# Kernel tuning notes

Hardware: AMD Instinct MI355X
Metric: run time of the kernel (lower is better)

Reference implementation:

```python
import jax, jax.numpy as jnp
import numpy as np

K = 3
LOSS_WEIGHT = 1.0
EPS_NORM = 1e-8
EPS_DIV = 1e-10


def setup_inputs() -> dict:
    key = jax.random.key(0)
    k1, k2, k3 = jax.random.split(key, 3)
    N = 32768          # total points over all segments
    NSEG = 8           # number of scenes (len(nums)); equal-size segments of 4096
    pred_ = jax.random.normal(k1, (N, 3), dtype=jnp.float32)
    coord = jax.random.uniform(k2, (N, 3), dtype=jnp.float32) * 10.0
    target = jax.random.normal(k3, (N, 3), dtype=jnp.float32)
    nums = jnp.arange(NSEG, dtype=jnp.int32)  # only len(nums) matters; segments are equal-sized
    return {"pred_": pred_, "coord": coord, "target": target, "nums": nums}


def _segment_loss(cp, pp, tp):
    # cp: (S,3) coords, pp: (S,3) normalized pred, tp: (S,3) target
    # squared euclidean distances via the ||x||^2 trick (monotone in distance,
    # so topk-smallest matches torch.cdist + topk(largest=False))
    sq = jnp.sum(cp * cp, axis=-1)                       # (S,)
    d2 = sq[:, None] + sq[None, :] - 2.0 * (cp @ cp.T)   # (S,S)
    S = cp.shape[0]
    eye = jnp.eye(S, dtype=bool)
    d2 = jnp.where(eye, -1.0, jnp.maximum(d2, 0.0))      # self always nearest
    _, idx = jax.lax.top_k(-d2, K + 1)                   # (S,K+1) smallest dists
    idx = idx[:, 1:]                                     # drop self -> (S,K)

    nbr = pp[idx]                                        # (S,K,3) gather
    sim = jnp.abs(jnp.sum(nbr * pp[:, None, :], axis=2))
    sim = jnp.clip(sim, -1.0, 1.0)

    tnbr = tp[idx]                                       # (S,K,3)
    tsim = jnp.abs(jnp.sum(tnbr * tp[:, None, :], axis=2))
    tsim = jnp.clip(tsim, -1.0, 1.0)

    return jnp.mean((sim - tsim) ** 2)                   # F.mse_loss(mean)


def reference(pred_, coord, target, nums):
    nseg = nums.shape[0]
    seg = pred_.shape[0] // nseg
    # normalize predicted directions
    inp = jnp.sqrt(jnp.sum(pred_ * pred_, axis=-1, keepdims=True) + EPS_NORM)
    pred_norm = pred_ / (inp + EPS_DIV)
    c = coord.reshape(nseg, seg, 3)
    p = pred_norm.reshape(nseg, seg, 3)
    t = target.reshape(nseg, seg, 3)
    losses = jax.vmap(_segment_loss)(c, p, t)            # (nseg,)
    return jnp.mean(losses) * LOSS_WEIGHT
```

## Files before the change

kernel.cpp:

```cpp
#include <hip/hip_runtime.h>
#include <math.h>

#define G 8
#define NCELL (G*G*G)
#define INV_CS 0.8f
#define CS 1.25f
#define KNN 3
#define BIGF 3.402823466e+38f

#define BUILD_BLOCK 1024
#define SEARCH_BLOCK 512
#define SPLIT 8
#define PTS_PER_SBLOCK (SEARCH_BLOCK / SPLIT)

__device__ __forceinline__ int cell_of(float x, float y, float z) {
    int cx = (int)(x * INV_CS); cx = cx < 0 ? 0 : (cx > G-1 ? G-1 : cx);
    int cy = (int)(y * INV_CS); cy = cy < 0 ? 0 : (cy > G-1 ? G-1 : cy);
    int cz = (int)(z * INV_CS); cz = cz < 0 ? 0 : (cz > G-1 ? G-1 : cz);
    return (cx << 6) | (cy << 3) | cz;
}

__device__ __forceinline__ void pk_insert(double pk, double& m0, double& m1, double& m2) {
    const double lo0 = fmin(m0, pk);
    const double hi0 = fmax(m0, pk);
    m0 = lo0;
    const double lo1 = fmin(m1, hi0);
    const double hi1 = fmax(m1, hi0);
    m1 = lo1;
    m2 = fmin(m2, hi1);
}

__global__ __launch_bounds__(BUILD_BLOCK) void build_grid(
    const float* __restrict__ coord,
    float4* __restrict__ sorted,
    int* __restrict__ cellstart,
    float* __restrict__ out,
    int seg)
{
    __shared__ int hist[NCELL];
    __shared__ int scanb[NCELL];
    __shared__ int start[NCELL + 1];

    const int tid = threadIdx.x;
    const int s   = blockIdx.x;
    const long segbase = (long)s * seg;

    if (s == 0 && tid == 0) out[0] = 0.0f;

    if (tid < NCELL) hist[tid] = 0;
    __syncthreads();

    for (int p = tid; p < seg; p += BUILD_BLOCK) {
        const float x = coord[(segbase + p)*3 + 0];
        const float y = coord[(segbase + p)*3 + 1];
        const float z = coord[(segbase + p)*3 + 2];
        atomicAdd(&hist[cell_of(x, y, z)], 1);
    }
    __syncthreads();

    if (tid < NCELL) scanb[tid] = hist[tid];
    __syncthreads();
    for (int off = 1; off < NCELL; off <<= 1) {
        int add = 0;
        if (tid < NCELL && tid >= off) add = scanb[tid - off];
        __syncthreads();
        if (tid < NCELL) scanb[tid] += add;
        __syncthreads();
    }
    if (tid < NCELL) {
        start[tid] = scanb[tid] - hist[tid];
        if (tid == NCELL - 1) start[NCELL] = scanb[tid];
    }
    __syncthreads();

    if (tid < NCELL) {
        cellstart[s * (NCELL + 1) + tid] = start[tid];
        if (tid == 0) cellstart[s * (NCELL + 1) + NCELL] = start[NCELL];
        hist[tid] = start[tid];
    }
    __syncthreads();

    for (int p = tid; p < seg; p += BUILD_BLOCK) {
        const float x = coord[(segbase + p)*3 + 0];
        const float y = coord[(segbase + p)*3 + 1];
        const float z = coord[(segbase + p)*3 + 2];
        const int c = cell_of(x, y, z);
        const int slot = atomicAdd(&hist[c], 1);
        sorted[segbase + slot] = make_float4(x, y, z, __int_as_float(p));
    }
}

__global__ __launch_bounds__(SEARCH_BLOCK) void knn_loss(
    const float4* __restrict__ sorted,
    const int* __restrict__ cellstart,
    const float* __restrict__ pred,
    const float* __restrict__ target,
    float* __restrict__ out,
    int seg, float inv_total)
{
    __shared__ int csl[NCELL + 1];
    __shared__ float wred[SEARCH_BLOCK / 64];

    const int tid = threadIdx.x;
    const int sub = tid & (SPLIT - 1);
    const int pt  = blockIdx.x * PTS_PER_SBLOCK + (tid >> 3);
    const int s   = pt >> 12;
    const int j   = pt & 4095;
    const long segbase = (long)s * seg;

    for (int i = tid; i < NCELL + 1; i += SEARCH_BLOCK)
        csl[i] = cellstart[s * (NCELL + 1) + i];
    __syncthreads();

    const float4 me = sorted[segbase + j];
    const int myorig = __float_as_int(me.w);
    const int cx = (me.x * INV_CS) > (float)(G-1) ? G-1 : (int)(me.x * INV_CS);
    const int cy = (me.y * INV_CS) > (float)(G-1) ? G-1 : (int)(me.y * INV_CS);
    const int cz = (me.z * INV_CS) > (float)(G-1) ? G-1 : (int)(me.z * INV_CS);

    const double BIGP = __hiloint2double(__float_as_int(BIGF), -1);
    double m0, m1, m2;
    int R = 1;
    for (;;) {
        m0 = BIGP; m1 = BIGP; m2 = BIGP;
        const int x0 = max(cx - R, 0), x1 = min(cx + R, G-1);
        const int y0 = max(cy - R, 0), y1 = min(cy + R, G-1);
        const int z0 = max(cz - R, 0), z1 = min(cz + R, G-1);
        for (int gx = x0; gx <= x1; ++gx) {
            for (int gy = y0; gy <= y1; ++gy) {
                const int base = (gx << 6) | (gy << 3);
                const int q0 = csl[base + z0];
                const int q1 = csl[base + z1 + 1];
                for (int q = q0 + sub; q < q1; q += SPLIT) {
                    const float4 c = sorted[segbase + q];
                    const float dx = me.x - c.x;
                    const float dy = me.y - c.y;
                    const float dz = me.z - c.z;
                    float d2 = fmaf(dx, dx, fmaf(dy, dy, dz * dz));
                    if (q == j) d2 = BIGF;
                    pk_insert(__hiloint2double(__float_as_int(d2),
                                               __float_as_int(c.w)),
                              m0, m1, m2);
                }
            }
        }
        #pragma unroll
        for (int mask = 1; mask < SPLIT; mask <<= 1) {
            const double o0 = __shfl_xor(m0, mask);
            const double o1 = __shfl_xor(m1, mask);
            const double o2 = __shfl_xor(m2, mask);
            pk_insert(o0, m0, m1, m2);
            pk_insert(o1, m0, m1, m2);
            pk_insert(o2, m0, m1, m2);
        }
        const float d3 = __uint_as_float((unsigned)__double2hiint(m2));
        const float g = (float)R * CS;
        if (d3 <= g * g || R >= G) break;
        ++R;
    }

    float loss = 0.0f;
    if (sub == 0) {
        const int nbr[KNN] = { __double2loint(m0), __double2loint(m1), __double2loint(m2) };

        const long gp = segbase + myorig;
        const float px = pred[gp*3+0], py = pred[gp*3+1], pz = pred[gp*3+2];
        const float inp = sqrtf(px*px + py*py + pz*pz + 1e-8f) + 1e-10f;
        const float qx = px / inp, qy = py / inp, qz = pz / inp;
        const float tx = target[gp*3+0], ty = target[gp*3+1], tz = target[gp*3+2];

        #pragma unroll
        for (int k = 0; k < KNN; ++k) {
            const long gn = segbase + nbr[k];
            const float nx = pred[gn*3+0], ny = pred[gn*3+1], nz = pred[gn*3+2];
            const float ninp = sqrtf(nx*nx + ny*ny + nz*nz + 1e-8f) + 1e-10f;
            float sim = fabsf((nx*qx + ny*qy + nz*qz) / ninp);
            sim = fminf(sim, 1.0f);
            const float ux = target[gn*3+0], uy = target[gn*3+1], uz = target[gn*3+2];
            float tsim = fabsf(ux*tx + uy*ty + uz*tz);
            tsim = fminf(tsim, 1.0f);
            const float diff = sim - tsim;
            loss += diff * diff;
        }
    }

    #pragma unroll
    for (int off = 32; off > 0; off >>= 1)
        loss += __shfl_down(loss, off);
    if ((tid & 63) == 0) wred[tid >> 6] = loss;
    __syncthreads();
    if (tid == 0) {
        float ssum = 0.0f;
        #pragma unroll
        for (int w = 0; w < SEARCH_BLOCK / 64; ++w) ssum += wred[w];
        atomicAdd(out, ssum * inv_total);
    }
}

extern "C" void kernel_launch(void* const* d_in, const int* in_sizes, int n_in,
                              void* d_out, int out_size, void* d_ws, size_t ws_size,
                              hipStream_t stream) {
    const float* pred   = (const float*)d_in[0];
    const float* coord  = (const float*)d_in[1];
    const float* target = (const float*)d_in[2];
    float* out = (float*)d_out;

    const int N    = in_sizes[0] / 3;
    const int nseg = in_sizes[3];
    const int seg  = N / nseg;

    float4* sorted  = (float4*)d_ws;
    int* cellstart  = (int*)((char*)d_ws + (size_t)N * sizeof(float4));

    build_grid<<<nseg, BUILD_BLOCK, 0, stream>>>(coord, sorted, cellstart, out, seg);

    const float inv_total = 1.0f / ((float)nseg * (float)seg * (float)KNN);
    knn_loss<<<N / PTS_PER_SBLOCK, SEARCH_BLOCK, 0, stream>>>(
        sorted, cellstart, pred, target, out, seg, inv_total);
}
```

Before: 81.00 us.

## Split grid build into parallel histogram, scan and scatter kernels

```diff
diff --git a/kernel.cpp b/kernel.cpp
--- a/kernel.cpp
+++ b/kernel.cpp
@@ -8,8 +8,9 @@
 #define KNN 3
 #define BIGF 3.402823466e+38f
 
-#define BUILD_BLOCK 1024
-#define SEARCH_BLOCK 512
+#define HIST_BLOCK 256
+#define SCAN_BLOCK 512
+#define SEARCH_BLOCK 256
 #define SPLIT 8
 #define PTS_PER_SBLOCK (SEARCH_BLOCK / SPLIT)
 
@@ -30,64 +31,63 @@
     m2 = fmin(m2, hi1);
 }
 
-__global__ __launch_bounds__(BUILD_BLOCK) void build_grid(
+__global__ __launch_bounds__(HIST_BLOCK) void hist_kernel(
     const float* __restrict__ coord,
-    float4* __restrict__ sorted,
+    int* __restrict__ pcell,
+    int* __restrict__ hist,
+    int N)
+{
+    const int p = blockIdx.x * HIST_BLOCK + threadIdx.x;
+    if (p >= N) return;
+    const int s = p >> 12;
+    const float x = coord[p*3 + 0];
+    const float y = coord[p*3 + 1];
+    const float z = coord[p*3 + 2];
+    const int c = cell_of(x, y, z);
+    pcell[p] = c;
+    atomicAdd(&hist[(s << 9) + c], 1);
+}
+
+__global__ __launch_bounds__(SCAN_BLOCK) void scan_kernel(
+    const int* __restrict__ hist,
     int* __restrict__ cellstart,
-    float* __restrict__ out,
-    int seg)
-{
-    __shared__ int hist[NCELL];
-    __shared__ int scanb[NCELL];
-    __shared__ int start[NCELL + 1];
-
+    int* __restrict__ cursor)
+{
+    __shared__ int sb[NCELL];
     const int tid = threadIdx.x;
     const int s   = blockIdx.x;
-    const long segbase = (long)s * seg;
-
-    if (s == 0 && tid == 0) out[0] = 0.0f;
-
-    if (tid < NCELL) hist[tid] = 0;
-    __syncthreads();
-
-    for (int p = tid; p < seg; p += BUILD_BLOCK) {
-        const float x = coord[(segbase + p)*3 + 0];
-        const float y = coord[(segbase + p)*3 + 1];
-        const float z = coord[(segbase + p)*3 + 2];
-        atomicAdd(&hist[cell_of(x, y, z)], 1);
-    }
-    __syncthreads();
-
-    if (tid < NCELL) scanb[tid] = hist[tid];
+    const int own = hist[(s << 9) + tid];
+    sb[tid] = own;
     __syncthreads();
     for (int off = 1; off < NCELL; off <<= 1) {
-        int add = 0;
-        if (tid < NCELL && tid >= off) add = scanb[tid - off];
+        const int add = (tid >= off) ? sb[tid - off] : 0;
         __syncthreads();
-        if (tid < NCELL) scanb[tid] += add;
+        sb[tid] += add;
         __syncthreads();
     }
-    if (tid < NCELL) {
-        start[tid] = scanb[tid] - hist[tid];
-        if (tid == NCELL - 1) start[NCELL] = scanb[tid];
-    }
-    __syncthreads();
-
-    if (tid < NCELL) {
-        cellstart[s * (NCELL + 1) + tid] = start[tid];
-        if (tid == 0) cellstart[s * (NCELL + 1) + NCELL] = start[NCELL];
-        hist[tid] = start[tid];
-    }
-    __syncthreads();
-
-    for (int p = tid; p < seg; p += BUILD_BLOCK) {
-        const float x = coord[(segbase + p)*3 + 0];
-        const float y = coord[(segbase + p)*3 + 1];
-        const float z = coord[(segbase + p)*3 + 2];
-        const int c = cell_of(x, y, z);
-        const int slot = atomicAdd(&hist[c], 1);
-        sorted[segbase + slot] = make_float4(x, y, z, __int_as_float(p));
-    }
+    const int excl = sb[tid] - own;
+    cellstart[s * (NCELL + 1) + tid] = excl;
+    cursor[(s << 9) + tid] = excl;
+    if (tid == NCELL - 1) cellstart[s * (NCELL + 1) + NCELL] = sb[tid];
+}
+
+__global__ __launch_bounds__(HIST_BLOCK) void scatter_kernel(
+    const float* __restrict__ coord,
+    const int* __restrict__ pcell,
+    int* __restrict__ cursor,
+    float4* __restrict__ sorted,
+    int N, int seg)
+{
+    const int p = blockIdx.x * HIST_BLOCK + threadIdx.x;
+    if (p >= N) return;
+    const int s = p >> 12;
+    const int c = pcell[p];
+    const float x = coord[p*3 + 0];
+    const float y = coord[p*3 + 1];
+    const float z = coord[p*3 + 2];
+    const int slot = atomicAdd(&cursor[(s << 9) + c], 1);
+    sorted[(long)s * seg + slot] =
+        make_float4(x, y, z, __int_as_float(p & (seg - 1)));
 }
 
 __global__ __launch_bounds__(SEARCH_BLOCK) void knn_loss(
@@ -209,10 +209,21 @@
     const int nseg = in_sizes[3];
     const int seg  = N / nseg;
 
-    float4* sorted  = (float4*)d_ws;
-    int* cellstart  = (int*)((char*)d_ws + (size_t)N * sizeof(float4));
-
-    build_grid<<<nseg, BUILD_BLOCK, 0, stream>>>(coord, sorted, cellstart, out, seg);
+    char* ws = (char*)d_ws;
+    float4* sorted   = (float4*)ws;                       ws += (size_t)N * sizeof(float4);
+    int* cellstart   = (int*)ws;                          ws += (size_t)nseg * (NCELL + 1) * sizeof(int);
+    ws = (char*)(((size_t)ws + 15) & ~(size_t)15);
+    int* cursor      = (int*)ws;                          ws += (size_t)nseg * NCELL * sizeof(int);
+    int* hist        = (int*)ws;                          ws += (size_t)nseg * NCELL * sizeof(int);
+    int* pcell       = (int*)ws;
+
+    hipMemsetAsync(hist, 0, (size_t)nseg * NCELL * sizeof(int), stream);
+    hipMemsetAsync(out, 0, sizeof(float), stream);
+
+    const int pblocks = (N + HIST_BLOCK - 1) / HIST_BLOCK;
+    hist_kernel<<<pblocks, HIST_BLOCK, 0, stream>>>(coord, pcell, hist, N);
+    scan_kernel<<<nseg, SCAN_BLOCK, 0, stream>>>(hist, cellstart, cursor);
+    scatter_kernel<<<pblocks, HIST_BLOCK, 0, stream>>>(coord, pcell, cursor, sorted, N, seg);
 
     const float inv_total = 1.0f / ((float)nseg * (float)seg * (float)KNN);
     knn_loss<<<N / PTS_PER_SBLOCK, SEARCH_BLOCK, 0, stream>>>(
```

Measured after the change: 93.01 us. +14.8%, slower.

## Fuse grid build into KNN kernel with per-block shared-memory cell sort

Applied to the files above, without the earlier changes.

```diff
diff --git a/kernel.cpp b/kernel.cpp
--- a/kernel.cpp
+++ b/kernel.cpp
@@ -8,10 +8,11 @@
 #define KNN 3
 #define BIGF 3.402823466e+38f
 
-#define BUILD_BLOCK 1024
-#define SEARCH_BLOCK 512
+#define BLOCK 512
 #define SPLIT 8
-#define PTS_PER_SBLOCK (SEARCH_BLOCK / SPLIT)
+#define PTS_PER_BLOCK (BLOCK / SPLIT)
+#define SEG 4096
+#define PPT (SEG / BLOCK)
 
 __device__ __forceinline__ int cell_of(float x, float y, float z) {
     int cx = (int)(x * INV_CS); cx = cx < 0 ? 0 : (cx > G-1 ? G-1 : cx);
@@ -30,93 +31,87 @@
     m2 = fmin(m2, hi1);
 }
 
-__global__ __launch_bounds__(BUILD_BLOCK) void build_grid(
+__global__ __launch_bounds__(BLOCK) void fused_knn_loss(
+    const float* __restrict__ pred,
     const float* __restrict__ coord,
-    float4* __restrict__ sorted,
-    int* __restrict__ cellstart,
-    float* __restrict__ out,
-    int seg)
-{
-    __shared__ int hist[NCELL];
-    __shared__ int scanb[NCELL];
-    __shared__ int start[NCELL + 1];
-
-    const int tid = threadIdx.x;
-    const int s   = blockIdx.x;
-    const long segbase = (long)s * seg;
-
-    if (s == 0 && tid == 0) out[0] = 0.0f;
-
-    if (tid < NCELL) hist[tid] = 0;
-    __syncthreads();
-
-    for (int p = tid; p < seg; p += BUILD_BLOCK) {
-        const float x = coord[(segbase + p)*3 + 0];
-        const float y = coord[(segbase + p)*3 + 1];
-        const float z = coord[(segbase + p)*3 + 2];
-        atomicAdd(&hist[cell_of(x, y, z)], 1);
-    }
-    __syncthreads();
-
-    if (tid < NCELL) scanb[tid] = hist[tid];
-    __syncthreads();
-    for (int off = 1; off < NCELL; off <<= 1) {
-        int add = 0;
-        if (tid < NCELL && tid >= off) add = scanb[tid - off];
-        __syncthreads();
-        if (tid < NCELL) scanb[tid] += add;
-        __syncthreads();
-    }
-    if (tid < NCELL) {
-        start[tid] = scanb[tid] - hist[tid];
-        if (tid == NCELL - 1) start[NCELL] = scanb[tid];
-    }
-    __syncthreads();
-
-    if (tid < NCELL) {
-        cellstart[s * (NCELL + 1) + tid] = start[tid];
-        if (tid == 0) cellstart[s * (NCELL + 1) + NCELL] = start[NCELL];
-        hist[tid] = start[tid];
-    }
-    __syncthreads();
-
-    for (int p = tid; p < seg; p += BUILD_BLOCK) {
-        const float x = coord[(segbase + p)*3 + 0];
-        const float y = coord[(segbase + p)*3 + 1];
-        const float z = coord[(segbase + p)*3 + 2];
-        const int c = cell_of(x, y, z);
-        const int slot = atomicAdd(&hist[c], 1);
-        sorted[segbase + slot] = make_float4(x, y, z, __int_as_float(p));
-    }
-}
-
-__global__ __launch_bounds__(SEARCH_BLOCK) void knn_loss(
-    const float4* __restrict__ sorted,
-    const int* __restrict__ cellstart,
-    const float* __restrict__ pred,
     const float* __restrict__ target,
     float* __restrict__ out,
-    int seg, float inv_total)
+    int seg, int bps,
+    float inv_total)
 {
-    __shared__ int csl[NCELL + 1];
-    __shared__ float wred[SEARCH_BLOCK / 64];
+    __shared__ float2 sxy[SEG];
+    __shared__ float  sz[SEG];
+    __shared__ unsigned short sid[SEG];
+    __shared__ int   csl[NCELL + 1];
+    __shared__ int   hist[NCELL];
+    __shared__ int   wsum[BLOCK / 64];
+    __shared__ float wred[BLOCK / 64];
 
     const int tid = threadIdx.x;
-    const int sub = tid & (SPLIT - 1);
-    const int pt  = blockIdx.x * PTS_PER_SBLOCK + (tid >> 3);
-    const int s   = pt >> 12;
-    const int j   = pt & 4095;
+    const int s   = blockIdx.x / bps;
     const long segbase = (long)s * seg;
 
-    for (int i = tid; i < NCELL + 1; i += SEARCH_BLOCK)
-        csl[i] = cellstart[s * (NCELL + 1) + i];
-    __syncthreads();
-
-    const float4 me = sorted[segbase + j];
-    const int myorig = __float_as_int(me.w);
-    const int cx = (me.x * INV_CS) > (float)(G-1) ? G-1 : (int)(me.x * INV_CS);
-    const int cy = (me.y * INV_CS) > (float)(G-1) ? G-1 : (int)(me.y * INV_CS);
-    const int cz = (me.z * INV_CS) > (float)(G-1) ? G-1 : (int)(me.z * INV_CS);
+    hist[tid] = 0;
+    __syncthreads();
+
+    float px[PPT], py[PPT], pz[PPT];
+    int   pc[PPT];
+    #pragma unroll
+    for (int k = 0; k < PPT; ++k) {
+        const int p = tid + k * BLOCK;
+        px[k] = coord[(segbase + p)*3 + 0];
+        py[k] = coord[(segbase + p)*3 + 1];
+        pz[k] = coord[(segbase + p)*3 + 2];
+        pc[k] = cell_of(px[k], py[k], pz[k]);
+        atomicAdd(&hist[pc[k]], 1);
+    }
+    __syncthreads();
+
+    const int own = hist[tid];
+    int v = own;
+    #pragma unroll
+    for (int off = 1; off < 64; off <<= 1) {
+        const int t = __shfl_up(v, off);
+        if ((tid & 63) >= off) v += t;
+    }
+    if ((tid & 63) == 63) wsum[tid >> 6] = v;
+    __syncthreads();
+    if (tid < 64) {
+        int w = (tid < 8) ? wsum[tid] : 0;
+        #pragma unroll
+        for (int off = 1; off < 8; off <<= 1) {
+            const int t = __shfl_up(w, off);
+            if (tid >= off) w += t;
+        }
+        if (tid < 8) wsum[tid] = w;
+    }
+    __syncthreads();
+    const int wid  = tid >> 6;
+    const int incl = v + (wid ? wsum[wid - 1] : 0);
+    const int excl = incl - own;
+    csl[tid] = excl;
+    if (tid == BLOCK - 1) csl[NCELL] = incl;
+    hist[tid] = excl;
+    __syncthreads();
+
+    #pragma unroll
+    for (int k = 0; k < PPT; ++k) {
+        const int slot = atomicAdd(&hist[pc[k]], 1);
+        sxy[slot] = make_float2(px[k], py[k]);
+        sz[slot]  = pz[k];
+        sid[slot] = (unsigned short)(tid + k * BLOCK);
+    }
+    __syncthreads();
+
+    const int sub   = tid & (SPLIT - 1);
+    const int grp   = tid >> 3;
+    const int jloc  = (blockIdx.x % bps) * PTS_PER_BLOCK + grp;
+    const float mx = coord[(segbase + jloc)*3 + 0];
+    const float my = coord[(segbase + jloc)*3 + 1];
+    const float mz = coord[(segbase + jloc)*3 + 2];
+    const int cx = (mx * INV_CS) > (float)(G-1) ? G-1 : (int)(mx * INV_CS);
+    const int cy = (my * INV_CS) > (float)(G-1) ? G-1 : (int)(my * INV_CS);
+    const int cz = (mz * INV_CS) > (float)(G-1) ? G-1 : (int)(mz * INV_CS);
 
     const double BIGP = __hiloint2double(__float_as_int(BIGF), -1);
     double m0, m1, m2;
@@ -132,14 +127,15 @@
                 const int q0 = csl[base + z0];
                 const int q1 = csl[base + z1 + 1];
                 for (int q = q0 + sub; q < q1; q += SPLIT) {
-                    const float4 c = sorted[segbase + q];
-                    const float dx = me.x - c.x;
-                    const float dy = me.y - c.y;
-                    const float dz = me.z - c.z;
+                    const float2 xy = sxy[q];
+                    const float  zz = sz[q];
+                    const int    id = sid[q];
+                    const float dx = mx - xy.x;
+                    const float dy = my - xy.y;
+                    const float dz = mz - zz;
                     float d2 = fmaf(dx, dx, fmaf(dy, dy, dz * dz));
-                    if (q == j) d2 = BIGF;
-                    pk_insert(__hiloint2double(__float_as_int(d2),
-                                               __float_as_int(c.w)),
+                    if (id == jloc) d2 = BIGF;
+                    pk_insert(__hiloint2double(__float_as_int(d2), id),
                               m0, m1, m2);
                 }
             }
@@ -162,11 +158,10 @@
     float loss = 0.0f;
     if (sub == 0) {
         const int nbr[KNN] = { __double2loint(m0), __double2loint(m1), __double2loint(m2) };
-
-        const long gp = segbase + myorig;
-        const float px = pred[gp*3+0], py = pred[gp*3+1], pz = pred[gp*3+2];
-        const float inp = sqrtf(px*px + py*py + pz*pz + 1e-8f) + 1e-10f;
-        const float qx = px / inp, qy = py / inp, qz = pz / inp;
+        const long gp = segbase + jloc;
+        const float ppx = pred[gp*3+0], ppy = pred[gp*3+1], ppz = pred[gp*3+2];
+        const float inp = sqrtf(ppx*ppx + ppy*ppy + ppz*ppz + 1e-8f) + 1e-10f;
+        const float qx = ppx / inp, qy = ppy / inp, qz = ppz / inp;
         const float tx = target[gp*3+0], ty = target[gp*3+1], tz = target[gp*3+2];
 
         #pragma unroll
@@ -192,7 +187,7 @@
     if (tid == 0) {
         float ssum = 0.0f;
         #pragma unroll
-        for (int w = 0; w < SEARCH_BLOCK / 64; ++w) ssum += wred[w];
+        for (int w = 0; w < BLOCK / 64; ++w) ssum += wred[w];
         atomicAdd(out, ssum * inv_total);
     }
 }
@@ -208,13 +203,11 @@
     const int N    = in_sizes[0] / 3;
     const int nseg = in_sizes[3];
     const int seg  = N / nseg;
-
-    float4* sorted  = (float4*)d_ws;
-    int* cellstart  = (int*)((char*)d_ws + (size_t)N * sizeof(float4));
-
-    build_grid<<<nseg, BUILD_BLOCK, 0, stream>>>(coord, sorted, cellstart, out, seg);
+    const int bps  = seg / PTS_PER_BLOCK;
+
+    hipMemsetAsync(out, 0, sizeof(float), stream);
 
     const float inv_total = 1.0f / ((float)nseg * (float)seg * (float)KNN);
-    knn_loss<<<N / PTS_PER_SBLOCK, SEARCH_BLOCK, 0, stream>>>(
-        sorted, cellstart, pred, target, out, seg, inv_total);
-}
+    fused_knn_loss<<<N / PTS_PER_BLOCK, BLOCK, 0, stream>>>(
+        pred, coord, target, out, seg, bps, inv_total);
+}
```

Result: faster. 78.74 us (-2.8%).
